# Kernel optimization log

Measured on AMD Instinct MI355X. Metric: run time of the kernel, lower is better.

Reference implementation:

```python
import jax, jax.numpy as jnp
import numpy as np

N = 20000   # nodes
E = 160000  # edges
D = 128     # out_dim == in_dim
H = 8       # heads
DK = D // H # 16


def setup_inputs() -> dict:
    key = jax.random.key(0)
    ks = jax.random.split(key, 16)
    f = lambda i, shape, s=1.0: jax.random.normal(ks[i], shape, dtype=jnp.float32) * s
    z = lambda shape: jnp.zeros(shape, dtype=jnp.float32)
    return {
        "x_txt": f(0, (N, D)), "x_img": f(1, (N, D)), "x_s": f(2, (N, D)),
        "Wk": f(3, (D, D), 0.05), "bk": z((D,)),
        "Wq": f(4, (D, D), 0.05), "bq": z((D,)),
        "Wv": f(5, (D, D), 0.05), "bv": z((D,)),
        "Wa": f(6, (D, D), 0.05), "ba": z((D,)),
        "rel_att": f(7, (H, DK, DK), 0.25),
        "rel_msg": f(8, (H, DK, DK), 0.25),
        "rel_pri": jnp.ones((H,), jnp.float32),
        "wm_txt": f(9, (H, DK, DK), 0.25),
        "wm_img": f(10, (H, DK, DK), 0.25),
        "wm_s": f(11, (H, DK, DK), 0.25),
        "skip": jnp.ones((1,), jnp.float32),
        "src": jax.random.randint(ks[12], (E,), 0, N),
        "dst": jax.random.randint(ks[13], (E,), 0, N),
    }


def reference(x_txt, x_img, x_s, Wk, bk, Wq, bq, Wv, bv, Wa, ba,
              rel_att, rel_msg, rel_pri, wm_txt, wm_img, wm_s, skip, src, dst):
    n_heads, dk = rel_att.shape[0], rel_att.shape[1]
    n_nodes = x_txt.shape[0]
    sqrt_dk = jnp.sqrt(jnp.asarray(dk, jnp.float32))

    def proj(x, W, b):
        return (x @ W + b).reshape(n_nodes, n_heads, dk)

    xs = (x_txt, x_img, x_s)
    k = [proj(x, Wk, bk)[src] for x in xs]  # [E,H,dk] gathered at src
    q = [proj(x, Wq, bq)[dst] for x in xs]  # [E,H,dk] gathered at dst
    v = [proj(x, Wv, bv)[src] for x in xs]

    # cross-modal lambda: per-edge modality alignment softmax (over the 3 modalities)
    wm = (wm_txt, wm_img, wm_s)
    lam_scores = jnp.stack(
        [jnp.einsum('ehd,hdf,ehf->eh', k[m], wm[m], q[m]) for m in range(3)], axis=0)
    lam = jax.nn.softmax(lam_scores, axis=0)  # [3,E,H]

    # edge attention logits (scaled *10 as in reduce_func) and relation-msg values
    att = [jnp.einsum('ehd,hdf,ehf->eh', k[m], rel_att, q[m]) * rel_pri / sqrt_dk * 10.0
           for m in range(3)]
    vmsg = [jnp.einsum('ehd,hdf->ehf', v[m], rel_msg) for m in range(3)]

    align = -(jnp.abs(att[0] - att[1]) + jnp.abs(att[0] - att[2])
              + jnp.abs(att[1] - att[2])) / 3.0

    def seg_softmax(x):  # softmax over edges sharing the same dst node
        m = jax.ops.segment_max(x, dst, num_segments=n_nodes)
        m = jnp.where(jnp.isfinite(m), m, 0.0)
        e = jnp.exp(x - m[dst])
        s = jax.ops.segment_sum(e, dst, num_segments=n_nodes)
        s = jnp.where(s == 0.0, 1.0, s)
        return e / s[dst]

    beta2 = seg_softmax(align)
    sm = [seg_softmax(a) for a in att]
    beta1 = sm[0] * lam[0] + sm[1] * lam[1] + sm[2] * lam[2]
    beta = seg_softmax(beta1 * beta2)  # [E,H]

    alpha = jax.nn.sigmoid(skip)  # [1]
    outs = []
    for m in range(3):
        h = jax.ops.segment_sum(beta[..., None] * vmsg[m], dst,
                                num_segments=n_nodes).reshape(n_nodes, -1)
        outs.append((h @ Wa + ba) * alpha + xs[m] * (1.0 - alpha))
    return tuple(outs)
```

## Files before the change

kernel.cpp:

```cpp
#include <hip/hip_runtime.h>

#define D 128
#define NH 8

typedef __bf16 bf16x8 __attribute__((ext_vector_type(8)));
typedef unsigned short ushortx8 __attribute__((ext_vector_type(8)));
typedef float floatx4 __attribute__((ext_vector_type(4)));

__device__ __forceinline__ float bf2f(unsigned short u) {
  union { unsigned int i; float f; } x; x.i = ((unsigned int)u) << 16; return x.f;
}
__device__ __forceinline__ unsigned short f2bf(float f) {
  union { float f; unsigned int i; } x; x.f = f;
  unsigned int i = x.i;
  return (unsigned short)((i + 0x7FFFu + ((i >> 16) & 1u)) >> 16);
}
__device__ __forceinline__ void acc2(unsigned int ku, unsigned int qu, float& s) {
  union { unsigned int i; float f; } a, b;
  a.i = ku << 16;          b.i = qu << 16;          s += a.f * b.f;
  a.i = ku & 0xffff0000u;  b.i = qu & 0xffff0000u;  s += a.f * b.f;
}

__device__ __forceinline__ void fold_item(
    int gid,
    const float* __restrict__ Wk, const float* __restrict__ bk,
    const float* __restrict__ Wq, const float* __restrict__ bq,
    const float* __restrict__ Wv, const float* __restrict__ bv,
    const float* __restrict__ rel_att, const float* __restrict__ rel_msg,
    const float* __restrict__ rel_pri,
    const float* __restrict__ wm0, const float* __restrict__ wm1,
    const float* __restrict__ wm2,
    unsigned short* __restrict__ Wt_all, float* __restrict__ bias_all)
{
  int p = gid >> 14;
  int idx = gid & 16383;
  int c = idx >> 7, k = idx & 127;
  int h = c >> 4, r = c & 15;
  float wsum = 0.f, bsum = 0.f;
  if (p == 0) {
    wsum = Wk[k * 128 + c];
    bsum = bk[c];
  } else if (p <= 4) {
    const float* M = (p == 1) ? rel_att : ((p == 2) ? wm0 : ((p == 3) ? wm1 : wm2));
#pragma unroll
    for (int f = 0; f < 16; f++) {
      float mv = M[h * 256 + r * 16 + f];
      wsum += Wq[k * 128 + h * 16 + f] * mv;
      bsum += bq[h * 16 + f] * mv;
    }
    if (p == 1) { float sc = rel_pri[h] * 2.5f; wsum *= sc; bsum *= sc; }
  } else {
#pragma unroll
    for (int d = 0; d < 16; d++) {
      float mv = rel_msg[h * 256 + d * 16 + r];
      wsum += Wv[k * 128 + h * 16 + d] * mv;
      bsum += bv[h * 16 + d] * mv;
    }
  }
  Wt_all[(size_t)p * 16384 + c * 128 + k] = f2bf(wsum);
  if (k == 0) bias_all[p * 128 + c] = bsum;
}

__device__ __forceinline__ void proj_tile(
    int t, const float* __restrict__ x0, const float* __restrict__ x1,
    const float* __restrict__ x2,
    const unsigned short* __restrict__ Wt_all, const float* __restrict__ bias_all,
    unsigned short* __restrict__ P, int N, unsigned short* Wt, int tid)
{
  int m = t % 3, rt = t / 3;
  const float* X = (m == 0) ? x0 : ((m == 1) ? x1 : x2);
  int wave = tid >> 6, lane = tid & 63;
  int quad = lane >> 4, l16 = lane & 15;
  int row0 = rt * 64 + wave * 16;
  int arow = row0 + l16; if (arow >= N) arow = N - 1;
  const float* ap = X + (size_t)arow * D;
  bf16x8 afr[4];
#pragma unroll
  for (int kk4 = 0; kk4 < 4; kk4++) {
    float4 f0 = *(const float4*)(ap + kk4 * 32 + quad * 8);
    float4 f1 = *(const float4*)(ap + kk4 * 32 + quad * 8 + 4);
    ushortx8 uu;
    uu[0]=f2bf(f0.x); uu[1]=f2bf(f0.y); uu[2]=f2bf(f0.z); uu[3]=f2bf(f0.w);
    uu[4]=f2bf(f1.x); uu[5]=f2bf(f1.y); uu[6]=f2bf(f1.z); uu[7]=f2bf(f1.w);
    afr[kk4] = __builtin_bit_cast(bf16x8, uu);
  }
  for (int pt = 0; pt < 4; pt++) {
    int wp = (pt == 0) ? 0 : ((pt == 1) ? 1 : ((pt == 2) ? (2 + m) : 5));
    const unsigned short* Wsrc = Wt_all + (size_t)wp * 16384;
    const float* B = bias_all + wp * 128;
    unsigned short* Pout = P + (size_t)(pt * 3 + m) * N * D;
    for (int half = 0; half < 2; half++) {
      __syncthreads();
#pragma unroll
      for (int it = 0; it < 4; it++) {
        int idx = it * 256 + tid;
        int c = idx >> 4, kc = (idx & 15) << 3;
        *(uint4*)(&Wt[c * 136 + kc]) =
            *(const uint4*)(&Wsrc[(half * 64 + c) * 128 + kc]);
      }
      __syncthreads();
      floatx4 acc[4];
#pragma unroll
      for (int ct = 0; ct < 4; ct++) acc[ct] = (floatx4)0.f;
#pragma unroll
      for (int kk4 = 0; kk4 < 4; kk4++) {
#pragma unroll
        for (int ct2 = 0; ct2 < 4; ct2++) {
          uint4 bu = *(const uint4*)(&Wt[(ct2 * 16 + l16) * 136 + kk4 * 32 + quad * 8]);
          bf16x8 bf = __builtin_bit_cast(bf16x8, bu);
          acc[ct2] =
              __builtin_amdgcn_mfma_f32_16x16x32_bf16(afr[kk4], bf, acc[ct2], 0, 0, 0);
        }
      }
#pragma unroll
      for (int ct2 = 0; ct2 < 4; ct2++) {
        int col = half * 64 + ct2 * 16 + l16;
        float bias = B[col];
#pragma unroll
        for (int i = 0; i < 4; i++) {
          int r = row0 + quad * 4 + i;
          if (r < N) Pout[(size_t)r * D + col] = f2bf(acc[ct2][i] + bias);
        }
      }
    }
  }
}

__device__ __forceinline__ void assign_chunk(
    int a, const int* __restrict__ counts, int* __restrict__ row_start,
    int* __restrict__ cursor, int* __restrict__ allocg, int N, int lane)
{
  int n = a * 64 + lane;
  int cnt = (n < N) ? counts[n] : 0;
  int x = cnt;
#pragma unroll
  for (int off = 1; off < 64; off <<= 1) {
    int y = __shfl_up(x, off, 64);
    if (lane >= off) x += y;
  }
  int wtot = __shfl(x, 63, 64);
  int wbase = 0;
  if (lane == 63) wbase = atomicAdd(allocg, wtot);
  wbase = __shfl(wbase, 63, 64);
  if (n < N) { int v = wbase + x - cnt; row_start[n] = v; cursor[n] = v; }
}

__device__ __forceinline__ void edge_vals(
    const unsigned short* __restrict__ P, size_t Nsz, int s, int h,
    const uint4 (&qa)[3][2], const uint4 (&qw)[3][2],
    float (&av)[3], float (&lv)[3])
{
#pragma unroll
  for (int m = 0; m < 3; m++) {
    const unsigned short* kp = P + ((size_t)m * Nsz + s) * 128 + h * 16;
    uint4 k0 = *(const uint4*)kp, k1 = *(const uint4*)(kp + 8);
    const unsigned int* ka = (const unsigned int*)&k0;
    const unsigned int* kb = (const unsigned int*)&k1;
    const unsigned int* a0 = (const unsigned int*)&qa[m][0];
    const unsigned int* a1 = (const unsigned int*)&qa[m][1];
    const unsigned int* w0 = (const unsigned int*)&qw[m][0];
    const unsigned int* w1 = (const unsigned int*)&qw[m][1];
    float da = 0.f, dw = 0.f;
#pragma unroll
    for (int j = 0; j < 4; j++) {
      acc2(ka[j], a0[j], da); acc2(kb[j], a1[j], da);
      acc2(ka[j], w0[j], dw); acc2(kb[j], w1[j], dw);
    }
    av[m] = da;
    lv[m] = dw;
  }
  float mx = fmaxf(lv[0], fmaxf(lv[1], lv[2]));
  float e0 = __expf(lv[0] - mx), e1 = __expf(lv[1] - mx), e2 = __expf(lv[2] - mx);
  float inv = 1.f / (e0 + e1 + e2);
  lv[0] = e0 * inv; lv[1] = e1 * inv; lv[2] = e2 * inv;
}

__device__ __forceinline__ void node_one(
    int n, const unsigned short* __restrict__ P,
    const int* __restrict__ row_start, const int* __restrict__ counts,
    const int* __restrict__ srcs, unsigned short* __restrict__ hagg,
    int N, int lane)
{
  int ro = row_start[n];
  int deg = counts[n];
  float acc00 = 0, acc01 = 0, acc10 = 0, acc11 = 0, acc20 = 0, acc21 = 0;
  if (deg > 0) {
    int h = lane & 7, slot = lane >> 3;
    size_t Nsz = (size_t)N;
    uint4 qa[3][2], qw[3][2];
#pragma unroll
    for (int m = 0; m < 3; m++) {
      const unsigned short* qap = P + ((size_t)(3 + m) * Nsz + n) * 128 + h * 16;
      const unsigned short* qwp = P + ((size_t)(6 + m) * Nsz + n) * 128 + h * 16;
      qa[m][0] = *(const uint4*)qap; qa[m][1] = *(const uint4*)(qap + 8);
      qw[m][0] = *(const uint4*)qwp; qw[m][1] = *(const uint4*)(qwp + 8);
    }
    int nch = (deg + 7) >> 3;
    float cX0[4] = {}, cX1[4] = {}, cX2[4] = {}, cEa[4] = {}, cT[4] = {};
    int cS[4] = {};
    float sA0 = 0, sA1 = 0, sA2 = 0, sAl = 0;
#pragma unroll
    for (int c = 0; c < 4; c++) {
      int idx = c * 8 + slot;
      if (c < nch && idx < deg) {
        int s = srcs[ro + idx]; cS[c] = s;
        float av[3], lv[3];
        edge_vals(P, Nsz, s, h, qa, qw, av, lv);
        float e0 = __expf(av[0]), e1 = __expf(av[1]), e2 = __expf(av[2]);
        float align = -(fabsf(av[0]-av[1]) + fabsf(av[0]-av[2]) + fabsf(av[1]-av[2])) * (1.f/3.f);
        float ea = __expf(align);
        cX0[c] = lv[0] * e0; cX1[c] = lv[1] * e1; cX2[c] = lv[2] * e2; cEa[c] = ea;
        sA0 += e0; sA1 += e1; sA2 += e2; sAl += ea;
      }
    }
    for (int c = 4; c < nch; c++) {
      int idx = c * 8 + slot;
      if (idx < deg) {
        int s = srcs[ro + idx];
        float av[3], lv[3];
        edge_vals(P, Nsz, s, h, qa, qw, av, lv);
        float align = -(fabsf(av[0]-av[1]) + fabsf(av[0]-av[2]) + fabsf(av[1]-av[2])) * (1.f/3.f);
        sA0 += __expf(av[0]); sA1 += __expf(av[1]); sA2 += __expf(av[2]);
        sAl += __expf(align);
      }
    }
#pragma unroll
    for (int off = 8; off < 64; off <<= 1) {
      sA0 += __shfl_xor(sA0, off, 64);
      sA1 += __shfl_xor(sA1, off, 64);
      sA2 += __shfl_xor(sA2, off, 64);
      sAl += __shfl_xor(sAl, off, 64);
    }
    float rA0 = 1.f / fmaxf(sA0, 1e-30f), rA1 = 1.f / fmaxf(sA1, 1e-30f);
    float rA2 = 1.f / fmaxf(sA2, 1e-30f), rAl = 1.f / fmaxf(sAl, 1e-30f);
    float sT = 0;
#pragma unroll
    for (int c = 0; c < 4; c++) {
      int idx = c * 8 + slot;
      if (c < nch && idx < deg) {
        float t = (cX0[c] * rA0 + cX1[c] * rA1 + cX2[c] * rA2) * (cEa[c] * rAl);
        cT[c] = t;
        sT += __expf(t);
      }
    }
    for (int c = 4; c < nch; c++) {
      int idx = c * 8 + slot;
      if (idx < deg) {
        int s = srcs[ro + idx];
        float av[3], lv[3];
        edge_vals(P, Nsz, s, h, qa, qw, av, lv);
        float align = -(fabsf(av[0]-av[1]) + fabsf(av[0]-av[2]) + fabsf(av[1]-av[2])) * (1.f/3.f);
        float t = (lv[0]*__expf(av[0])*rA0 + lv[1]*__expf(av[1])*rA1 + lv[2]*__expf(av[2])*rA2)
                  * (__expf(align) * rAl);
        sT += __expf(t);
      }
    }
#pragma unroll
    for (int off = 8; off < 64; off <<= 1) sT += __shfl_xor(sT, off, 64);
    float rT = 1.f / fmaxf(sT, 1e-30f);
    const unsigned int* Pu = (const unsigned int*)P;
    int hl = lane >> 3;
#pragma unroll
    for (int c = 0; c < 4; c++) {
      if (c < nch) {
        int idx = c * 8 + slot;
        float beta = (idx < deg) ? __expf(cT[c]) * rT : 0.f;
        int sv = cS[c];
        float bj[8]; int sj[8];
#pragma unroll
        for (int jj = 0; jj < 8; jj++) {
          bj[jj] = __shfl(beta, jj * 8 + hl, 64);
          sj[jj] = __shfl(sv, jj * 8, 64);
        }
#pragma unroll
        for (int jj = 0; jj < 8; jj++) {
          size_t base9 = ((size_t)9 * Nsz + sj[jj]) * 64 + lane;
          unsigned int u0 = Pu[base9];
          unsigned int u1 = Pu[base9 + Nsz * 64];
          unsigned int u2 = Pu[base9 + 2 * Nsz * 64];
          float b = bj[jj];
          acc00 += b * bf2f((unsigned short)u0); acc01 += b * bf2f((unsigned short)(u0 >> 16));
          acc10 += b * bf2f((unsigned short)u1); acc11 += b * bf2f((unsigned short)(u1 >> 16));
          acc20 += b * bf2f((unsigned short)u2); acc21 += b * bf2f((unsigned short)(u2 >> 16));
        }
      }
    }
    for (int c = 4; c < nch; c++) {
      int idx = c * 8 + slot;
      float beta = 0.f; int sv = 0;
      if (idx < deg) {
        sv = srcs[ro + idx];
        float av[3], lv[3];
        edge_vals(P, Nsz, sv, h, qa, qw, av, lv);
        float align = -(fabsf(av[0]-av[1]) + fabsf(av[0]-av[2]) + fabsf(av[1]-av[2])) * (1.f/3.f);
        float t = (lv[0]*__expf(av[0])*rA0 + lv[1]*__expf(av[1])*rA1 + lv[2]*__expf(av[2])*rA2)
                  * (__expf(align) * rAl);
        beta = __expf(t) * rT;
      }
      int jmax = min(8, deg - c * 8);
      for (int jj = 0; jj < jmax; jj++) {
        float b = __shfl(beta, jj * 8 + hl, 64);
        int s = __shfl(sv, jj * 8, 64);
        size_t base9 = ((size_t)9 * Nsz + s) * 64 + lane;
        unsigned int u0 = Pu[base9];
        unsigned int u1 = Pu[base9 + Nsz * 64];
        unsigned int u2 = Pu[base9 + 2 * Nsz * 64];
        acc00 += b * bf2f((unsigned short)u0); acc01 += b * bf2f((unsigned short)(u0 >> 16));
        acc10 += b * bf2f((unsigned short)u1); acc11 += b * bf2f((unsigned short)(u1 >> 16));
        acc20 += b * bf2f((unsigned short)u2); acc21 += b * bf2f((unsigned short)(u2 >> 16));
      }
    }
  }
  unsigned int* ho = (unsigned int*)hagg;
  ho[((size_t)0 * N + n) * 64 + lane] = ((unsigned int)f2bf(acc01) << 16) | f2bf(acc00);
  ho[((size_t)1 * N + n) * 64 + lane] = ((unsigned int)f2bf(acc11) << 16) | f2bf(acc10);
  ho[((size_t)2 * N + n) * 64 + lane] = ((unsigned int)f2bf(acc21) << 16) | f2bf(acc20);
}

__device__ __forceinline__ void out_tile_half(
    int t, int half, const unsigned short* __restrict__ Hagg,
    const float* __restrict__ ba,
    const float* __restrict__ x0, const float* __restrict__ x1,
    const float* __restrict__ x2, float alpha,
    float* __restrict__ out, int N, const unsigned short* Wt, int tid)
{
  int m = t % 3, rt = t / 3;
  const float* X = (m == 0) ? x0 : ((m == 1) ? x1 : x2);
  float oma = 1.f - alpha;
  int wave = tid >> 6, lane = tid & 63;
  int quad = lane >> 4, l16 = lane & 15;
  int row0 = rt * 64 + wave * 16;
  int arow = row0 + l16; if (arow >= N) arow = N - 1;
  const unsigned short* hp = Hagg + ((size_t)m * N + arow) * D;
  floatx4 acc[4];
#pragma unroll
  for (int ct = 0; ct < 4; ct++) acc[ct] = (floatx4)0.f;
#pragma unroll
  for (int kk = 0; kk < 128; kk += 32) {
    uint4 au = *(const uint4*)(hp + kk + quad * 8);
    bf16x8 af = __builtin_bit_cast(bf16x8, au);
#pragma unroll
    for (int ct = 0; ct < 4; ct++) {
      uint4 bu = *(const uint4*)(&Wt[(ct * 16 + l16) * 136 + kk + quad * 8]);
      bf16x8 bf = __builtin_bit_cast(bf16x8, bu);
      acc[ct] = __builtin_amdgcn_mfma_f32_16x16x32_bf16(af, bf, acc[ct], 0, 0, 0);
    }
  }
  float* om = out + (size_t)m * N * D;
#pragma unroll
  for (int ct = 0; ct < 4; ct++) {
    int col = half * 64 + ct * 16 + l16;
    float bias = ba[col];
#pragma unroll
    for (int i = 0; i < 4; i++) {
      int r = row0 + quad * 4 + i;
      if (r < N) {
        om[(size_t)r * D + col] =
            (acc[ct][i] + bias) * alpha + X[(size_t)r * D + col] * oma;
      }
    }
  }
}

__global__ __launch_bounds__(256) void fb_misc(
    const float* Wk, const float* bk, const float* Wq, const float* bq,
    const float* Wv, const float* bv,
    const float* rel_att, const float* rel_msg, const float* rel_pri,
    const float* wm0, const float* wm1, const float* wm2,
    unsigned short* Wt_all, float* bias_all,
    const int* dst, int* counts, int E)
{
  int b = blockIdx.x;
  if (b < 384) {
    int g = b * 256 + threadIdx.x;
    if (g < 6 * 16384)
      fold_item(g, Wk, bk, Wq, bq, Wv, bv, rel_att, rel_msg, rel_pri,
                wm0, wm1, wm2, Wt_all, bias_all);
  } else {
    int e = (b - 384) * 256 + threadIdx.x;
    if (e < E) atomicAdd(&counts[dst[e]], 1);
  }
}

__global__ __launch_bounds__(256) void fb_projassign(
    const float* x0, const float* x1, const float* x2,
    const unsigned short* Wt_all, const float* bias_all,
    unsigned short* P, const int* counts, int* row_start, int* cursor,
    int* allocg, int N)
{
  __shared__ __attribute__((aligned(16))) unsigned short Wt[64 * 136];
  int ntiles = ((N + 63) / 64) * 3;
  int b = blockIdx.x;
  if (b < ntiles) {
    proj_tile(b, x0, x1, x2, Wt_all, bias_all, P, N, Wt, threadIdx.x);
  } else {
    int a = (b - ntiles) * 4 + (threadIdx.x >> 6);
    if (a < (N + 63) / 64)
      assign_chunk(a, counts, row_start, cursor, allocg, N, threadIdx.x & 63);
  }
}

__global__ void fb_scatter(const int* dst, const int* src, int* cursor,
                           int* src_sorted, int E) {
  int e = blockIdx.x * 256 + threadIdx.x;
  if (e < E) {
    int d = dst[e];
    int pos = atomicAdd(&cursor[d], 1);
    src_sorted[pos] = src[e];
  }
}

__global__ __launch_bounds__(256) void fb_node(
    const unsigned short* P, const int* row_start, const int* counts,
    const int* srcs, unsigned short* hagg, int N)
{
  int n = blockIdx.x * 4 + (threadIdx.x >> 6);
  if (n < N) node_one(n, P, row_start, counts, srcs, hagg, N, threadIdx.x & 63);
}

__global__ __launch_bounds__(256) void fb_out(
    const unsigned short* Hagg, const float* Wa, const float* ba,
    const float* x0, const float* x1, const float* x2, const float* skip,
    float* out, int N)
{
  __shared__ __attribute__((aligned(16))) unsigned short Wt[64 * 136];
  int tid = threadIdx.x;
  float alpha = 1.f / (1.f + __expf(-skip[0]));
  for (int half = 0; half < 2; half++) {
    __syncthreads();
#pragma unroll
    for (int it = 0; it < 8; it++) {
      int idx = it * 256 + tid;
      int k = idx >> 4;
      int c4 = (idx & 15) << 2;
      float4 w = *(const float4*)(&Wa[k * 128 + half * 64 + c4]);
      Wt[(c4 + 0) * 136 + k] = f2bf(w.x);
      Wt[(c4 + 1) * 136 + k] = f2bf(w.y);
      Wt[(c4 + 2) * 136 + k] = f2bf(w.z);
      Wt[(c4 + 3) * 136 + k] = f2bf(w.w);
    }
    __syncthreads();
    out_tile_half(blockIdx.x, half, Hagg, ba, x0, x1, x2, alpha, out, N, Wt, tid);
  }
}

extern "C" void kernel_launch(void* const* d_in, const int* in_sizes, int n_in,
                              void* d_out, int out_size, void* d_ws, size_t ws_size,
                              hipStream_t stream) {
  const float* x0 = (const float*)d_in[0];
  const float* x1 = (const float*)d_in[1];
  const float* x2 = (const float*)d_in[2];
  const float* Wk = (const float*)d_in[3];
  const float* bk = (const float*)d_in[4];
  const float* Wq = (const float*)d_in[5];
  const float* bq = (const float*)d_in[6];
  const float* Wv = (const float*)d_in[7];
  const float* bv = (const float*)d_in[8];
  const float* Wa = (const float*)d_in[9];
  const float* ba = (const float*)d_in[10];
  const float* rel_att = (const float*)d_in[11];
  const float* rel_msg = (const float*)d_in[12];
  const float* rel_pri = (const float*)d_in[13];
  const float* wm0 = (const float*)d_in[14];
  const float* wm1 = (const float*)d_in[15];
  const float* wm2 = (const float*)d_in[16];
  const float* skip = (const float*)d_in[17];
  const int* src = (const int*)d_in[18];
  const int* dstv = (const int*)d_in[19];
  int N = in_sizes[0] / D;
  int E = in_sizes[18];

  char* wsb = (char*)d_ws;
  size_t off = 0;
  auto alloc_b = [&](size_t bytes) { size_t o = off; off += (bytes + 63) & ~(size_t)63; return o; };
  unsigned short* P         = (unsigned short*)(wsb + alloc_b((size_t)12 * N * D * 2));
  unsigned short* Wt_all    = (unsigned short*)(wsb + alloc_b((size_t)6 * 16384 * 2));
  float*          bias_all  = (float*)(wsb + alloc_b((size_t)6 * 128 * 4));
  int*            ctrl      = (int*)(wsb + alloc_b(((size_t)144 + 2 * N) * 4));
  int*            row_start = (int*)(wsb + alloc_b((size_t)(N + 1) * 4));
  int*            src_sorted= (int*)(wsb + alloc_b((size_t)E * 4));
  unsigned short* hagg      = (unsigned short*)(wsb + alloc_b((size_t)3 * N * D * 2));
  int* allocg = ctrl + 128;
  int* counts = ctrl + 144;
  int* cursor = ctrl + 144 + N;

  hipMemsetAsync(ctrl, 0, ((size_t)144 + N) * sizeof(int), stream);

  int ntiles = ((N + 63) / 64) * 3;
  int nchunks = (N + 63) / 64;
  fb_misc<<<dim3(384 + (E + 255) / 256), 256, 0, stream>>>(
      Wk, bk, Wq, bq, Wv, bv, rel_att, rel_msg, rel_pri, wm0, wm1, wm2,
      Wt_all, bias_all, dstv, counts, E);
  fb_projassign<<<dim3(ntiles + (nchunks + 3) / 4), 256, 0, stream>>>(
      x0, x1, x2, Wt_all, bias_all, P, counts, row_start, cursor, allocg, N);
  fb_scatter<<<dim3((E + 255) / 256), 256, 0, stream>>>(
      dstv, src, cursor, src_sorted, E);
  fb_node<<<dim3((N + 3) / 4), 256, 0, stream>>>(
      P, row_start, counts, src_sorted, hagg, N);
  fb_out<<<dim3(ntiles), 256, 0, stream>>>(
      hagg, Wa, ba, x0, x1, x2, skip, (float*)d_out, N);
}
```

Before: 248.6 us.

## Interleave K and V projections per source node for contiguous gathers

Changes the projection output layout: K for the three modalities is stored contiguously per node (node-major, 384 bf16), and V is interleaved so each lane reads one 16-byte uint4 holding all three modalities instead of three scattered 4-byte loads. Q stays modality-major because it is read once per destination node. This targets the random per-edge gathers in the node kernel, replacing several cache lines per source node with fewer, contiguous ones. The cost is a padded V buffer (4 slots for 3 modalities) and strided, scattered 2-byte stores in the projection epilogue.

```diff
diff --git a/kernel.cpp b/kernel.cpp
--- a/kernel.cpp
+++ b/kernel.cpp
@@ -65,7 +65,9 @@
     int t, const float* __restrict__ x0, const float* __restrict__ x1,
     const float* __restrict__ x2,
     const unsigned short* __restrict__ Wt_all, const float* __restrict__ bias_all,
-    unsigned short* __restrict__ P, int N, unsigned short* Wt, int tid)
+    unsigned short* __restrict__ Pk, unsigned short* __restrict__ Pq,
+    unsigned short* __restrict__ Pv,
+    int N, unsigned short* Wt, int tid)
 {
   int m = t % 3, rt = t / 3;
   const float* X = (m == 0) ? x0 : ((m == 1) ? x1 : x2);
@@ -88,7 +90,6 @@
     int wp = (pt == 0) ? 0 : ((pt == 1) ? 1 : ((pt == 2) ? (2 + m) : 5));
     const unsigned short* Wsrc = Wt_all + (size_t)wp * 16384;
     const float* B = bias_all + wp * 128;
-    unsigned short* Pout = P + (size_t)(pt * 3 + m) * N * D;
     for (int half = 0; half < 2; half++) {
       __syncthreads();
 #pragma unroll
@@ -119,7 +120,16 @@
 #pragma unroll
         for (int i = 0; i < 4; i++) {
           int r = row0 + quad * 4 + i;
-          if (r < N) Pout[(size_t)r * D + col] = f2bf(acc[ct2][i] + bias);
+          if (r < N) {
+            unsigned short v = f2bf(acc[ct2][i] + bias);
+            if (pt == 0) {
+              Pk[((size_t)r * 3 + m) * 128 + col] = v;
+            } else if (pt == 3) {
+              Pv[(((size_t)r * 64 + (col >> 1)) * 4 + m) * 2 + (col & 1)] = v;
+            } else {
+              Pq[(size_t)((pt - 1) * 3 + m) * N * 128 + (size_t)r * 128 + col] = v;
+            }
+          }
         }
       }
     }
@@ -146,13 +156,14 @@
 }
 
 __device__ __forceinline__ void edge_vals(
-    const unsigned short* __restrict__ P, size_t Nsz, int s, int h,
+    const unsigned short* __restrict__ Pk, int s, int h,
     const uint4 (&qa)[3][2], const uint4 (&qw)[3][2],
     float (&av)[3], float (&lv)[3])
 {
+  const unsigned short* krow = Pk + (size_t)s * 384;
 #pragma unroll
   for (int m = 0; m < 3; m++) {
-    const unsigned short* kp = P + ((size_t)m * Nsz + s) * 128 + h * 16;
+    const unsigned short* kp = krow + m * 128 + h * 16;
     uint4 k0 = *(const uint4*)kp, k1 = *(const uint4*)(kp + 8);
     const unsigned int* ka = (const unsigned int*)&k0;
     const unsigned int* kb = (const unsigned int*)&k1;
@@ -176,7 +187,8 @@
 }
 
 __device__ __forceinline__ void node_one(
-    int n, const unsigned short* __restrict__ P,
+    int n, const unsigned short* __restrict__ Pk,
+    const unsigned short* __restrict__ Pq, const unsigned short* __restrict__ Pv,
     const int* __restrict__ row_start, const int* __restrict__ counts,
     const int* __restrict__ srcs, unsigned short* __restrict__ hagg,
     int N, int lane)
@@ -190,8 +202,8 @@
     uint4 qa[3][2], qw[3][2];
 #pragma unroll
     for (int m = 0; m < 3; m++) {
-      const unsigned short* qap = P + ((size_t)(3 + m) * Nsz + n) * 128 + h * 16;
-      const unsigned short* qwp = P + ((size_t)(6 + m) * Nsz + n) * 128 + h * 16;
+      const unsigned short* qap = Pq + ((size_t)m * Nsz + n) * 128 + h * 16;
+      const unsigned short* qwp = Pq + ((size_t)(3 + m) * Nsz + n) * 128 + h * 16;
       qa[m][0] = *(const uint4*)qap; qa[m][1] = *(const uint4*)(qap + 8);
       qw[m][0] = *(const uint4*)qwp; qw[m][1] = *(const uint4*)(qwp + 8);
     }
@@ -205,7 +217,7 @@
       if (c < nch && idx < deg) {
         int s = srcs[ro + idx]; cS[c] = s;
         float av[3], lv[3];
-        edge_vals(P, Nsz, s, h, qa, qw, av, lv);
+        edge_vals(Pk, s, h, qa, qw, av, lv);
         float e0 = __expf(av[0]), e1 = __expf(av[1]), e2 = __expf(av[2]);
         float align = -(fabsf(av[0]-av[1]) + fabsf(av[0]-av[2]) + fabsf(av[1]-av[2])) * (1.f/3.f);
         float ea = __expf(align);
@@ -218,7 +230,7 @@
       if (idx < deg) {
         int s = srcs[ro + idx];
         float av[3], lv[3];
-        edge_vals(P, Nsz, s, h, qa, qw, av, lv);
+        edge_vals(Pk, s, h, qa, qw, av, lv);
         float align = -(fabsf(av[0]-av[1]) + fabsf(av[0]-av[2]) + fabsf(av[1]-av[2])) * (1.f/3.f);
         sA0 += __expf(av[0]); sA1 += __expf(av[1]); sA2 += __expf(av[2]);
         sAl += __expf(align);
@@ -248,7 +260,7 @@
       if (idx < deg) {
         int s = srcs[ro + idx];
         float av[3], lv[3];
-        edge_vals(P, Nsz, s, h, qa, qw, av, lv);
+        edge_vals(Pk, s, h, qa, qw, av, lv);
         float align = -(fabsf(av[0]-av[1]) + fabsf(av[0]-av[2]) + fabsf(av[1]-av[2])) * (1.f/3.f);
         float t = (lv[0]*__expf(av[0])*rA0 + lv[1]*__expf(av[1])*rA1 + lv[2]*__expf(av[2])*rA2)
                   * (__expf(align) * rAl);
@@ -258,7 +270,7 @@
 #pragma unroll
     for (int off = 8; off < 64; off <<= 1) sT += __shfl_xor(sT, off, 64);
     float rT = 1.f / fmaxf(sT, 1e-30f);
-    const unsigned int* Pu = (const unsigned int*)P;
+    const uint4* Pv4 = (const uint4*)Pv;
     int hl = lane >> 3;
 #pragma unroll
     for (int c = 0; c < 4; c++) {
@@ -274,14 +286,11 @@
         }
 #pragma unroll
         for (int jj = 0; jj < 8; jj++) {
-          size_t base9 = ((size_t)9 * Nsz + sj[jj]) * 64 + lane;
-          unsigned int u0 = Pu[base9];
-          unsigned int u1 = Pu[base9 + Nsz * 64];
-          unsigned int u2 = Pu[base9 + 2 * Nsz * 64];
+          uint4 v4 = Pv4[(size_t)sj[jj] * 64 + lane];
           float b = bj[jj];
-          acc00 += b * bf2f((unsigned short)u0); acc01 += b * bf2f((unsigned short)(u0 >> 16));
-          acc10 += b * bf2f((unsigned short)u1); acc11 += b * bf2f((unsigned short)(u1 >> 16));
-          acc20 += b * bf2f((unsigned short)u2); acc21 += b * bf2f((unsigned short)(u2 >> 16));
+          acc00 += b * bf2f((unsigned short)v4.x); acc01 += b * bf2f((unsigned short)(v4.x >> 16));
+          acc10 += b * bf2f((unsigned short)v4.y); acc11 += b * bf2f((unsigned short)(v4.y >> 16));
+          acc20 += b * bf2f((unsigned short)v4.z); acc21 += b * bf2f((unsigned short)(v4.z >> 16));
         }
       }
     }
@@ -291,7 +300,7 @@
       if (idx < deg) {
         sv = srcs[ro + idx];
         float av[3], lv[3];
-        edge_vals(P, Nsz, sv, h, qa, qw, av, lv);
+        edge_vals(Pk, sv, h, qa, qw, av, lv);
         float align = -(fabsf(av[0]-av[1]) + fabsf(av[0]-av[2]) + fabsf(av[1]-av[2])) * (1.f/3.f);
         float t = (lv[0]*__expf(av[0])*rA0 + lv[1]*__expf(av[1])*rA1 + lv[2]*__expf(av[2])*rA2)
                   * (__expf(align) * rAl);
@@ -301,13 +310,10 @@
       for (int jj = 0; jj < jmax; jj++) {
         float b = __shfl(beta, jj * 8 + hl, 64);
         int s = __shfl(sv, jj * 8, 64);
-        size_t base9 = ((size_t)9 * Nsz + s) * 64 + lane;
-        unsigned int u0 = Pu[base9];
-        unsigned int u1 = Pu[base9 + Nsz * 64];
-        unsigned int u2 = Pu[base9 + 2 * Nsz * 64];
-        acc00 += b * bf2f((unsigned short)u0); acc01 += b * bf2f((unsigned short)(u0 >> 16));
-        acc10 += b * bf2f((unsigned short)u1); acc11 += b * bf2f((unsigned short)(u1 >> 16));
-        acc20 += b * bf2f((unsigned short)u2); acc21 += b * bf2f((unsigned short)(u2 >> 16));
+        uint4 v4 = Pv4[(size_t)s * 64 + lane];
+        acc00 += b * bf2f((unsigned short)v4.x); acc01 += b * bf2f((unsigned short)(v4.x >> 16));
+        acc10 += b * bf2f((unsigned short)v4.y); acc11 += b * bf2f((unsigned short)(v4.y >> 16));
+        acc20 += b * bf2f((unsigned short)v4.z); acc21 += b * bf2f((unsigned short)(v4.z >> 16));
       }
     }
   }
@@ -385,14 +391,15 @@
 __global__ __launch_bounds__(256) void fb_projassign(
     const float* x0, const float* x1, const float* x2,
     const unsigned short* Wt_all, const float* bias_all,
-    unsigned short* P, const int* counts, int* row_start, int* cursor,
+    unsigned short* Pk, unsigned short* Pq, unsigned short* Pv,
+    const int* counts, int* row_start, int* cursor,
     int* allocg, int N)
 {
   __shared__ __attribute__((aligned(16))) unsigned short Wt[64 * 136];
   int ntiles = ((N + 63) / 64) * 3;
   int b = blockIdx.x;
   if (b < ntiles) {
-    proj_tile(b, x0, x1, x2, Wt_all, bias_all, P, N, Wt, threadIdx.x);
+    proj_tile(b, x0, x1, x2, Wt_all, bias_all, Pk, Pq, Pv, N, Wt, threadIdx.x);
   } else {
     int a = (b - ntiles) * 4 + (threadIdx.x >> 6);
     if (a < (N + 63) / 64)
@@ -411,11 +418,12 @@
 }
 
 __global__ __launch_bounds__(256) void fb_node(
-    const unsigned short* P, const int* row_start, const int* counts,
+    const unsigned short* Pk, const unsigned short* Pq, const unsigned short* Pv,
+    const int* row_start, const int* counts,
     const int* srcs, unsigned short* hagg, int N)
 {
   int n = blockIdx.x * 4 + (threadIdx.x >> 6);
-  if (n < N) node_one(n, P, row_start, counts, srcs, hagg, N, threadIdx.x & 63);
+  if (n < N) node_one(n, Pk, Pq, Pv, row_start, counts, srcs, hagg, N, threadIdx.x & 63);
 }
 
 __global__ __launch_bounds__(256) void fb_out(
@@ -473,7 +481,9 @@
   char* wsb = (char*)d_ws;
   size_t off = 0;
   auto alloc_b = [&](size_t bytes) { size_t o = off; off += (bytes + 63) & ~(size_t)63; return o; };
-  unsigned short* P         = (unsigned short*)(wsb + alloc_b((size_t)12 * N * D * 2));
+  unsigned short* Pk        = (unsigned short*)(wsb + alloc_b((size_t)3 * N * D * 2));
+  unsigned short* Pq        = (unsigned short*)(wsb + alloc_b((size_t)6 * N * D * 2));
+  unsigned short* Pv        = (unsigned short*)(wsb + alloc_b((size_t)N * 64 * 4 * 4));
   unsigned short* Wt_all    = (unsigned short*)(wsb + alloc_b((size_t)6 * 16384 * 2));
   float*          bias_all  = (float*)(wsb + alloc_b((size_t)6 * 128 * 4));
   int*            ctrl      = (int*)(wsb + alloc_b(((size_t)144 + 2 * N) * 4));
@@ -492,11 +502,11 @@
       Wk, bk, Wq, bq, Wv, bv, rel_att, rel_msg, rel_pri, wm0, wm1, wm2,
       Wt_all, bias_all, dstv, counts, E);
   fb_projassign<<<dim3(ntiles + (nchunks + 3) / 4), 256, 0, stream>>>(
-      x0, x1, x2, Wt_all, bias_all, P, counts, row_start, cursor, allocg, N);
+      x0, x1, x2, Wt_all, bias_all, Pk, Pq, Pv, counts, row_start, cursor, allocg, N);
   fb_scatter<<<dim3((E + 255) / 256), 256, 0, stream>>>(
       dstv, src, cursor, src_sorted, E);
   fb_node<<<dim3((N + 3) / 4), 256, 0, stream>>>(
-      P, row_start, counts, src_sorted, hagg, N);
+      Pk, Pq, Pv, row_start, counts, src_sorted, hagg, N);
   fb_out<<<dim3(ntiles), 256, 0, stream>>>(
       hagg, Wa, ba, x0, x1, x2, skip, (float*)d_out, N);
 }
```

Measured after the change: 253.2 us. About the same (+1.9%).
